# Optimization experiments

Measured on AMD Instinct MI355X. Metric: run time of the kernel, lower is better.

Reference implementation:

```python
import jax, jax.numpy as jnp
import numpy as np

BN_EPS = 1e-5

def _bn_relu(x, gamma, beta):
    # x: [B, C, N]; BatchNorm1d in training mode: stats over (B, N) per channel
    mean = jnp.mean(x, axis=(0, 2), keepdims=True)
    var = jnp.var(x, axis=(0, 2), keepdims=True)
    xn = (x - mean) * jax.lax.rsqrt(var + BN_EPS)
    return jax.nn.relu(xn * gamma[None, :, None] + beta[None, :, None])


def setup_inputs() -> dict:
    key = jax.random.key(0)
    ks = jax.random.split(key, 8)
    B, N, S, D1, D2 = 16, 4096, 1024, 64, 256
    C_in, H = D1 + D2, 256  # mlp_list = [320, 256, 256]
    inp = {
        "xyz1": jax.random.normal(ks[0], (B, 3, N), jnp.float32),
        "xyz2": jax.random.normal(ks[1], (B, 3, S), jnp.float32),
        "points1": jax.random.normal(ks[2], (B, D1, N), jnp.float32),
        "points2": jax.random.normal(ks[3], (B, D2, S), jnp.float32),
        # 1x1 Conv1d weights of the SeqLinear pointNet MLP
        "W1": jax.random.normal(ks[4], (H, C_in), jnp.float32) / np.sqrt(C_in),
        "b1": jnp.zeros((H,), jnp.float32),
        "g1": jnp.ones((H,), jnp.float32),
        "bt1": jnp.zeros((H,), jnp.float32),
        "W2": jax.random.normal(ks[5], (H, H), jnp.float32) / np.sqrt(H),
        "b2": jnp.zeros((H,), jnp.float32),
        "g2": jnp.ones((H,), jnp.float32),
        "bt2": jnp.zeros((H,), jnp.float32),
    }
    return inp


def reference(xyz1, xyz2, points1, points2, W1, b1, g1, bt1, W2, b2, g2, bt2):
    x1 = jnp.transpose(xyz1, (0, 2, 1))   # [B, N, 3]
    x2 = jnp.transpose(xyz2, (0, 2, 1))   # [B, S, 3]
    p2 = jnp.transpose(points2, (0, 2, 1))  # [B, S, D2]
    B, N, _ = x1.shape

    # square_distance: ||x1||^2 + ||x2||^2 - 2 x1.x2  -> [B, N, S]
    dists = (jnp.sum(x1 * x1, axis=-1, keepdims=True)
             + jnp.sum(x2 * x2, axis=-1)[:, None, :]
             - 2.0 * jnp.einsum('bnc,bsc->bns', x1, x2))

    # 3 nearest neighbors (smallest distances)
    neg_d3, idx = jax.lax.top_k(-dists, 3)   # [B, N, 3]
    d3 = -neg_d3
    recip = 1.0 / (d3 + 1e-8)
    weight = recip / jnp.sum(recip, axis=2, keepdims=True)  # [B, N, 3]

    # gather neighbor features: [B, N, 3, D2]
    gathered = jax.vmap(lambda p, i: p[i])(p2, idx)
    interp = jnp.sum(gathered * weight[..., None], axis=2)  # [B, N, D2]

    new_points = jnp.concatenate([jnp.transpose(points1, (0, 2, 1)), interp], axis=-1)
    x = jnp.transpose(new_points, (0, 2, 1))  # [B, 320, N]

    # pointNet MLP: conv1x1 -> BN -> ReLU, twice
    h = jnp.einsum('oc,bcn->bon', W1, x) + b1[None, :, None]
    h = _bn_relu(h, g1, bt1)
    h = jnp.einsum('oc,bcn->bon', W2, h) + b2[None, :, None]
    h = _bn_relu(h, g2, bt2)
    return h
```

## Files before the change

### kernel.cpp

```cpp
#include <hip/hip_runtime.h>
#include <cstddef>

#define B_   16
#define N_   4096
#define S_   1024
#define D1_  64
#define D2_  256
#define CIN_ 320
#define H_   256
#define CH_  8
#define SC_  (S_ / CH_)
#define P_   (B_ * (N_ / 128))

using short8 = __attribute__((ext_vector_type(8))) short;
using f32x4  = __attribute__((ext_vector_type(4))) float;

typedef const __attribute__((address_space(1))) unsigned g1u32;
typedef __attribute__((address_space(3))) unsigned l3u32;

__device__ __forceinline__ void gl_lds16(const void* g, void* l) {
  __builtin_amdgcn_global_load_lds((g1u32*)g, (l3u32*)l, 16, 0, 0);
}

__device__ __forceinline__ float relu_f(float v) { return fmaxf(v, 0.0f); }

__device__ __forceinline__ ushort f2bf(float f) {
  unsigned u = __builtin_bit_cast(unsigned, f);
  u += 0x7fffu + ((u >> 16) & 1u);
  return (ushort)(u >> 16);
}
__device__ __forceinline__ unsigned f2bf2(float a, float b) {
  unsigned r;
  asm("v_cvt_pk_bf16_f32 %0, %1, %2" : "=v"(r) : "v"(a), "v"(b));
  return r;
}
__device__ __forceinline__ float bf2f(ushort u) {
  return __builtin_bit_cast(float, (unsigned)u << 16);
}

__global__ __launch_bounds__(256) void prep_knn(
    const float* __restrict__ points2, const float* __restrict__ W1,
    const float* __restrict__ W2, const float* __restrict__ xyz1,
    const float* __restrict__ xyz2, ushort* __restrict__ p2tb,
    ushort* __restrict__ W1b, ushort* __restrict__ W2b,
    float* __restrict__ pd, int* __restrict__ pi) {
  __shared__ union { float tile[32][33]; float4 P[SC_]; } sm;
  int g = blockIdx.x, t = threadIdx.x;
  if (g < 4096) {
    int z = g >> 8, rem = g & 255;
    int c0 = (rem & 31) * 32;
    int r0 = (rem >> 5) * 32;
    const float* in = points2 + (size_t)z * D2_ * S_;
    ushort* out = p2tb + (size_t)z * S_ * D2_;
    int tx = t & 31, ty = t >> 5;
#pragma unroll
    for (int j = 0; j < 4; ++j) {
      int r = r0 + ty + j * 8;
      sm.tile[ty + j * 8][tx] = in[(size_t)r * S_ + c0 + tx];
    }
    __syncthreads();
#pragma unroll
    for (int j = 0; j < 4; ++j) {
      int c = c0 + ty + j * 8;
      out[(size_t)c * D2_ + r0 + tx] = f2bf(sm.tile[tx][ty + j * 8]);
    }
  } else if (g < 4168) {
    int g2 = g - 4096;
    const float* src = (g2 < 40) ? W1 : W2;
    ushort* dst = (g2 < 40) ? W1b : W2b;
    int base = ((g2 < 40) ? g2 : g2 - 40) * 2048 + t * 8;
    float4 a = *(const float4*)&src[base];
    float4 b = *(const float4*)&src[base + 4];
    short8 r;
    ((unsigned*)&r)[0] = f2bf2(a.x, a.y);
    ((unsigned*)&r)[1] = f2bf2(a.z, a.w);
    ((unsigned*)&r)[2] = f2bf2(b.x, b.y);
    ((unsigned*)&r)[3] = f2bf2(b.z, b.w);
    *(short8*)&dst[base] = r;
  } else {
    int gk = g - 4168;
    int b = gk & 15;
    int ch = (gk >> 4) & 7;
    int n = (gk >> 7) * 256 + t;
    const float* x2b = xyz2 + (size_t)b * 3 * S_ + ch * SC_;
    if (t < SC_) {
      float x = x2b[t], y = x2b[S_ + t], z = x2b[2 * S_ + t];
      sm.P[t] = make_float4(-2.f * x, -2.f * y, -2.f * z, x * x + y * y + z * z);
    }
    __syncthreads();

    const float* x1b = xyz1 + (size_t)b * 3 * N_;
    float px = x1b[n], py = x1b[N_ + n], pz = x1b[2 * N_ + n];
    float sq1 = px * px + py * py + pz * pz;

    float d0 = 1e30f, d1 = 1e30f, d2 = 1e30f;
    int i0 = 0, i1 = 0, i2 = 0;
#pragma unroll 4
    for (int s = 0; s < SC_; ++s) {
      float4 p = sm.P[s];
      float d = fmaf(px, p.x, fmaf(py, p.y, fmaf(pz, p.z, p.w)));
      int gi = ch * SC_ + s;
      if (d < d2) {
        if (d < d1) {
          if (d < d0) { d2 = d1; i2 = i1; d1 = d0; i1 = i0; d0 = d; i0 = gi; }
          else        { d2 = d1; i2 = i1; d1 = d;  i1 = gi; }
        } else        { d2 = d;  i2 = gi; }
      }
    }
    size_t base = (((size_t)b * N_ + n) * CH_ + ch) * 3;
    pd[base] = d0 + sq1; pd[base + 1] = d1 + sq1; pd[base + 2] = d2 + sq1;
    pi[base] = i0; pi[base + 1] = i1; pi[base + 2] = i2;
  }
}

__global__ __launch_bounds__(256) void build_fused(
    const float* __restrict__ points1,
    const ushort* __restrict__ p2tb,
    const float* __restrict__ pd, const int* __restrict__ pi,
    ushort* __restrict__ xt) {
  __shared__ int   lidx[16][3];
  __shared__ float lw[16][3];
  __shared__ ushort p1t[16][72];
  int g = blockIdx.x, t = threadIdx.x;
  int b = g & 15;
  int p0 = (g >> 4) * 16;

  if (t < 16) {
    size_t pb = (size_t)b * N_ + p0 + t;
    const float* pdp = pd + pb * 24;
    const int*   pip = pi + pb * 24;
    float d0 = 1e30f, d1 = 1e30f, d2 = 1e30f;
    int i0 = 0, i1 = 0, i2 = 0;
#pragma unroll
    for (int k = 0; k < 24; ++k) {
      float d = pdp[k];
      int gi = pip[k];
      if (d < d2) {
        if (d < d1) {
          if (d < d0) { d2 = d1; i2 = i1; d1 = d0; i1 = i0; d0 = d; i0 = gi; }
          else        { d2 = d1; i2 = i1; d1 = d;  i1 = gi; }
        } else        { d2 = d;  i2 = gi; }
      }
    }
    float r0 = 1.0f / (d0 + 1e-8f);
    float r1 = 1.0f / (d1 + 1e-8f);
    float r2 = 1.0f / (d2 + 1e-8f);
    float rs = 1.0f / (r0 + r1 + r2);
    lidx[t][0] = i0; lidx[t][1] = i1; lidx[t][2] = i2;
    lw[t][0] = r0 * rs; lw[t][1] = r1 * rs; lw[t][2] = r2 * rs;
  }

  {
    int c = t >> 2, q4 = t & 3;
    float4 v = *(const float4*)&points1[((size_t)b * D1_ + c) * N_ + p0 + q4 * 4];
    p1t[q4 * 4 + 0][c] = f2bf(v.x);
    p1t[q4 * 4 + 1][c] = f2bf(v.y);
    p1t[q4 * 4 + 2][c] = f2bf(v.z);
    p1t[q4 * 4 + 3][c] = f2bf(v.w);
  }
  __syncthreads();

  int pl = t >> 4, q = t & 15;
  size_t pb = (size_t)b * N_ + p0 + pl;
  int i0 = lidx[pl][0], i1 = lidx[pl][1], i2 = lidx[pl][2];
  float w0 = lw[pl][0], w1 = lw[pl][1], w2 = lw[pl][2];
  const ushort* R0 = p2tb + ((size_t)b * S_ + i0) * D2_;
  const ushort* R1 = p2tb + ((size_t)b * S_ + i1) * D2_;
  const ushort* R2 = p2tb + ((size_t)b * S_ + i2) * D2_;
  ushort* o = xt + pb * CIN_;

  if (q < 8)
    *(short8*)(o + q * 8) = *(const short8*)&p1t[pl][q * 8];

#pragma unroll
  for (int it = 0; it < 2; ++it) {
    int c = it * 16 + q;
    short8 a = *(const short8*)&R0[c * 8];
    short8 d = *(const short8*)&R1[c * 8];
    short8 e = *(const short8*)&R2[c * 8];
    short8 r;
#pragma unroll
    for (int u = 0; u < 4; ++u) {
      float v0 = w0 * bf2f((ushort)a[2 * u]) + w1 * bf2f((ushort)d[2 * u]) +
                 w2 * bf2f((ushort)e[2 * u]);
      float v1 = w0 * bf2f((ushort)a[2 * u + 1]) + w1 * bf2f((ushort)d[2 * u + 1]) +
                 w2 * bf2f((ushort)e[2 * u + 1]);
      ((unsigned*)&r)[u] = f2bf2(v0, v1);
    }
    *(short8*)(o + D1_ + c * 8) = r;
  }
}

template <int K, bool BNIN>
__global__ __launch_bounds__(256) void gemm_pipe(
    const ushort* __restrict__ Wb, const ushort* __restrict__ Xt,
    const float* __restrict__ bias, const float* __restrict__ scin,
    const float* __restrict__ shin, ushort* __restrict__ Yt,
    float* __restrict__ ps1, float* __restrict__ ps2) {
  constexpr int NT = K / 64;
  __shared__ union SM {
    struct { ushort A[2][128][64]; ushort Bt[2][128][64]; } st;
    struct { ushort C[128][132]; float S1[128][33]; float S2[128][33]; } ep;
  } sm;
  __shared__ float scs_l[H_], shs_l[H_];

  int b  = blockIdx.z;
  int n0 = blockIdx.x * 128;
  int m0 = blockIdx.y * 128;
  int tid = threadIdx.x;
  int lane = tid & 63, wid = tid >> 6;
  int wm = (wid >> 1) * 64, wn = (wid & 1) * 64;
  int lr = lane & 15, hi = lane >> 4;
  size_t bn0 = (size_t)b * N_ + n0;

  if (BNIN) {
    for (int i = tid; i < K; i += 256) { scs_l[i] = scin[i]; shs_l[i] = shin[i]; }
  }

  const char* Agb = (const char*)(Wb + (size_t)m0 * K);
  const ushort* Bg = Xt + bn0 * K;
  const char* Bgb = (const char*)Bg;
  const size_t rowB = (size_t)K * 2;

  size_t gsrc[4];
  int    ldst[4];
  int    brow[4], bcol[4];
#pragma unroll
  for (int r = 0; r < 4; ++r) {
    int m = (wid * 4 + r) * 64 + lane;
    int row = m >> 3;
    int c = ((m & 7) - row) & 7;
    gsrc[r] = (size_t)row * rowB + (size_t)c * 16;
    ldst[r] = m * 16;
    brow[r] = row; bcol[r] = c;
  }

  auto stageA = [&](int buf, int kc) {
    char* bA = (char*)sm.st.A[buf];
    size_t kb = (size_t)kc * 128;
#pragma unroll
    for (int r = 0; r < 4; ++r)
      gl_lds16(Agb + gsrc[r] + kb, bA + ldst[r]);
  };
  auto stageB_dma = [&](int buf, int kc) {
    char* bB = (char*)sm.st.Bt[buf];
    size_t kb = (size_t)kc * 128;
#pragma unroll
    for (int r = 0; r < 4; ++r)
      gl_lds16(Bgb + gsrc[r] + kb, bB + ldst[r]);
  };

  short8 braw[4];
  auto loadB = [&](int kc) {
#pragma unroll
    for (int r = 0; r < 4; ++r)
      braw[r] = *(const short8*)&Bg[(size_t)brow[r] * K + kc * 64 + bcol[r] * 8];
  };
  auto writeB = [&](int buf, int kc) {
#pragma unroll
    for (int r = 0; r < 4; ++r) {
      int kb = kc * 64 + bcol[r] * 8;
      short8 pk;
#pragma unroll
      for (int u = 0; u < 4; ++u) {
        float y0 = relu_f(bf2f((ushort)braw[r][2 * u]) * scs_l[kb + 2 * u] +
                          shs_l[kb + 2 * u]);
        float y1 = relu_f(bf2f((ushort)braw[r][2 * u + 1]) * scs_l[kb + 2 * u + 1] +
                          shs_l[kb + 2 * u + 1]);
        ((unsigned*)&pk)[u] = f2bf2(y0, y1);
      }
      *(short8*)((char*)sm.st.Bt[buf] + ldst[r]) = pk;
    }
  };

  f32x4 acc[4][4] = {};

  stageA(0, 0);
  if (BNIN) {
    loadB(0);
    __syncthreads();
    writeB(0, 0);
  } else {
    stageB_dma(0, 0);
  }
  __syncthreads();

  int cur = 0;
  for (int t = 0; t < NT; ++t) {
    if (t + 1 < NT) {
      stageA(cur ^ 1, t + 1);
      if (BNIN) loadB(t + 1); else stageB_dma(cur ^ 1, t + 1);
    }
#pragma unroll
    for (int ks = 0; ks < 2; ++ks) {
      short8 af[4], bv[4];
#pragma unroll
      for (int i = 0; i < 4; ++i) {
        int rA = wm + i * 16 + lr;
        int rB = wn + i * 16 + lr;
        int sA = (rA + ks * 4 + hi) & 7;
        int sB = (rB + ks * 4 + hi) & 7;
        af[i] = *(const short8*)&sm.st.A[cur][rA][sA * 8];
        bv[i] = *(const short8*)&sm.st.Bt[cur][rB][sB * 8];
      }
#pragma unroll
      for (int mf = 0; mf < 4; ++mf)
#pragma unroll
        for (int nf = 0; nf < 4; ++nf)
          acc[mf][nf] = __builtin_amdgcn_mfma_f32_16x16x32_bf16(
              af[mf], bv[nf], acc[mf][nf], 0, 0, 0);
    }
    if (BNIN && t + 1 < NT) writeB(cur ^ 1, t + 1);
    __syncthreads();
    cur ^= 1;
  }

  float sum1[4][4] = {}, sum2[4][4] = {};
#pragma unroll
  for (int mf = 0; mf < 4; ++mf) {
#pragma unroll
    for (int nf = 0; nf < 4; ++nf) {
      int n = wn + nf * 16 + lr;
      float v[4];
#pragma unroll
      for (int j = 0; j < 4; ++j) {
        v[j] = acc[mf][nf][j] + bias[m0 + wm + mf * 16 + hi * 4 + j];
        sum1[mf][j] += v[j];
        sum2[mf][j] += v[j] * v[j];
      }
      ushort4 u;
      ((unsigned*)&u)[0] = f2bf2(v[0], v[1]);
      ((unsigned*)&u)[1] = f2bf2(v[2], v[3]);
      *(ushort4*)&sm.ep.C[n][wm + mf * 16 + hi * 4] = u;
    }
  }
  __syncthreads();
  {
    int rown = tid >> 4, q = tid & 15;
#pragma unroll
    for (int p = 0; p < 8; ++p) {
      int n = p * 16 + rown;
      short8 val = *(const short8*)&sm.ep.C[n][q * 8];
      *(short8*)&Yt[(bn0 + n) * H_ + m0 + q * 8] = val;
    }
  }
  int col = (wid & 1) * 16 + lr;
#pragma unroll
  for (int mf = 0; mf < 4; ++mf)
#pragma unroll
    for (int j = 0; j < 4; ++j) {
      int c = wm + mf * 16 + hi * 4 + j;
      sm.ep.S1[c][col] = sum1[mf][j];
      sm.ep.S2[c][col] = sum2[mf][j];
    }
  __syncthreads();
  int pidx = b * gridDim.x + blockIdx.x;
  int c = tid & 127;
  float s = 0.f;
  if (tid < 128) {
#pragma unroll
    for (int k = 0; k < 32; ++k) s += sm.ep.S1[c][k];
    ps1[(size_t)pidx * H_ + m0 + c] = s;
  } else {
#pragma unroll
    for (int k = 0; k < 32; ++k) s += sm.ep.S2[c][k];
    ps2[(size_t)pidx * H_ + m0 + c] = s;
  }
}

__global__ __launch_bounds__(256) void bn_stats_fin(
    const float* __restrict__ ps1, const float* __restrict__ ps2,
    const float* __restrict__ gamma, const float* __restrict__ beta,
    float* __restrict__ sc, float* __restrict__ sh) {
  int c = blockIdx.x, t = threadIdx.x;
  float s1 = ps1[(size_t)t * H_ + c] + ps1[(size_t)(t + 256) * H_ + c];
  float s2 = ps2[(size_t)t * H_ + c] + ps2[(size_t)(t + 256) * H_ + c];
  __shared__ float S1[256], S2[256];
  S1[t] = s1; S2[t] = s2;
  __syncthreads();
  for (int off = 128; off > 0; off >>= 1) {
    if (t < off) { S1[t] += S1[t + off]; S2[t] += S2[t + off]; }
    __syncthreads();
  }
  if (t == 0) {
    const float inv = 1.0f / (float)(B_ * N_);
    float mean = S1[0] * inv;
    float var  = S2[0] * inv - mean * mean;
    float g    = gamma[c] * rsqrtf(var + 1e-5f);
    sc[c] = g;
    sh[c] = beta[c] - mean * g;
  }
}

__global__ __launch_bounds__(256) void bn_out_t(
    const ushort* __restrict__ Hb, const float* __restrict__ sc,
    const float* __restrict__ sh, float* __restrict__ out) {
  __shared__ float tile[32][132];
  int b = blockIdx.z;
  int n0 = blockIdx.x * 32, m0 = blockIdx.y * 128;
  int t = threadIdx.x;
  int m8 = (t & 15) * 8;
  f32x4 sa = *(const f32x4*)&sc[m0 + m8];
  f32x4 sb = *(const f32x4*)&sc[m0 + m8 + 4];
  f32x4 ha = *(const f32x4*)&sh[m0 + m8];
  f32x4 hb = *(const f32x4*)&sh[m0 + m8 + 4];
  size_t bn0 = (size_t)b * N_ + n0;
#pragma unroll
  for (int pass = 0; pass < 2; ++pass) {
    int n = pass * 16 + (t >> 4);
    short8 v = *(const short8*)&Hb[(bn0 + n) * H_ + m0 + m8];
#pragma unroll
    for (int e = 0; e < 4; ++e) {
      tile[n][m8 + e]     = relu_f(bf2f((ushort)v[e]) * sa[e] + ha[e]);
      tile[n][m8 + 4 + e] = relu_f(bf2f((ushort)v[e + 4]) * sb[e] + hb[e]);
    }
  }
  __syncthreads();
  int m = t >> 1, nh = (t & 1) * 16;
  float* orow = out + ((size_t)b * H_ + m0 + m) * N_ + n0 + nh;
#pragma unroll
  for (int j = 0; j < 4; ++j) {
    float4 v;
    v.x = tile[nh + j * 4 + 0][m];
    v.y = tile[nh + j * 4 + 1][m];
    v.z = tile[nh + j * 4 + 2][m];
    v.w = tile[nh + j * 4 + 3][m];
    *(float4*)&orow[j * 4] = v;
  }
}

extern "C" void kernel_launch(void* const* d_in, const int* in_sizes, int n_in,
                              void* d_out, int out_size, void* d_ws,
                              size_t ws_size, hipStream_t stream) {
  const float* xyz1    = (const float*)d_in[0];
  const float* xyz2    = (const float*)d_in[1];
  const float* points1 = (const float*)d_in[2];
  const float* points2 = (const float*)d_in[3];
  const float* W1  = (const float*)d_in[4];
  const float* b1  = (const float*)d_in[5];
  const float* g1  = (const float*)d_in[6];
  const float* bt1 = (const float*)d_in[7];
  const float* W2  = (const float*)d_in[8];
  const float* b2  = (const float*)d_in[9];
  const float* g2  = (const float*)d_in[10];
  const float* bt2 = (const float*)d_in[11];
  float* out = (float*)d_out;
  char* cur = (char*)d_ws;
  auto alloc = [&](size_t bytes) { char* p = cur; cur += (bytes + 255) & ~255ull; return p; };

  ushort* p2tb = (ushort*)alloc((size_t)B_ * S_ * D2_ * 2);
  float*  pd   = (float*)alloc((size_t)B_ * N_ * CH_ * 3 * 4);
  int*    pi   = (int*)alloc((size_t)B_ * N_ * CH_ * 3 * 4);
  ushort* W1b  = (ushort*)alloc((size_t)H_ * CIN_ * 2);
  ushort* W2b  = (ushort*)alloc((size_t)H_ * H_ * 2);
  ushort* xct  = (ushort*)alloc((size_t)B_ * N_ * CIN_ * 2);
  ushort* h1t  = (ushort*)alloc((size_t)B_ * N_ * H_ * 2);
  float*  ps1  = (float*)alloc((size_t)P_ * H_ * 4);
  float*  ps2  = (float*)alloc((size_t)P_ * H_ * 4);
  float*  sc1  = (float*)alloc(H_ * 4);
  float*  sh1  = (float*)alloc(H_ * 4);
  float*  sc2  = (float*)alloc(H_ * 4);
  float*  sh2  = (float*)alloc(H_ * 4);
  ushort* h2b  = xct;

  prep_knn<<<4096 + 40 + 32 + 2048, 256, 0, stream>>>(
      points2, W1, W2, xyz1, xyz2, p2tb, W1b, W2b, pd, pi);

  build_fused<<<B_ * N_ / 16, 256, 0, stream>>>(points1, p2tb, pd, pi, xct);

  gemm_pipe<CIN_, false><<<dim3(N_ / 128, H_ / 128, B_), 256, 0, stream>>>(
      W1b, xct, b1, nullptr, nullptr, h1t, ps1, ps2);
  bn_stats_fin<<<H_, 256, 0, stream>>>(ps1, ps2, g1, bt1, sc1, sh1);

  gemm_pipe<H_, true><<<dim3(N_ / 128, H_ / 128, B_), 256, 0, stream>>>(
      W2b, h1t, b2, sc1, sh1, h2b, ps1, ps2);
  bn_stats_fin<<<H_, 256, 0, stream>>>(ps1, ps2, g2, bt2, sc2, sh2);

  bn_out_t<<<dim3(N_ / 32, H_ / 128, B_), 256, 0, stream>>>(h2b, sc2, sh2, out);
}
```

Baseline: 154.7 us.

## Apply W1 to source features before interpolation and fuse gather into first GEMM

Since interpolation is linear, the change multiplies the D2 slice of W1 with points2 once per source point (S=1024 rows instead of N=4096) to form Z, then in a new fused kernel computes W1a·points1 with MFMA and adds the weighted three-neighbour sum of Z rows in the epilogue. This drops the separate build kernel and the large concatenated bf16 intermediate, cutting GEMM1 FLOPs and memory traffic. It adds an extra bf16 rounding of Z before interpolation, and switches grids to flat 1D indexing with batch as the fastest-varying index.

```diff
diff --git a/kernel.cpp b/kernel.cpp
--- a/kernel.cpp
+++ b/kernel.cpp
@@ -42,8 +42,8 @@
     const float* __restrict__ points2, const float* __restrict__ W1,
     const float* __restrict__ W2, const float* __restrict__ xyz1,
     const float* __restrict__ xyz2, ushort* __restrict__ p2tb,
-    ushort* __restrict__ W1b, ushort* __restrict__ W2b,
-    float* __restrict__ pd, int* __restrict__ pi) {
+    ushort* __restrict__ W1a, ushort* __restrict__ W1z,
+    ushort* __restrict__ W2b, float* __restrict__ pd, int* __restrict__ pi) {
   __shared__ union { float tile[32][33]; float4 P[SC_]; } sm;
   int g = blockIdx.x, t = threadIdx.x;
   if (g < 4096) {
@@ -66,17 +66,32 @@
     }
   } else if (g < 4168) {
     int g2 = g - 4096;
-    const float* src = (g2 < 40) ? W1 : W2;
-    ushort* dst = (g2 < 40) ? W1b : W2b;
-    int base = ((g2 < 40) ? g2 : g2 - 40) * 2048 + t * 8;
-    float4 a = *(const float4*)&src[base];
-    float4 b = *(const float4*)&src[base + 4];
+    const float* s;
+    ushort* dst;
+    int e;
+    if (g2 < 8) {
+      e = g2 * 2048 + t * 8;
+      int row = e >> 6, col = e & 63;
+      s = W1 + (size_t)row * CIN_ + col;
+      dst = W1a;
+    } else if (g2 < 40) {
+      e = (g2 - 8) * 2048 + t * 8;
+      int row = e >> 8, col = e & 255;
+      s = W1 + (size_t)row * CIN_ + 64 + col;
+      dst = W1z;
+    } else {
+      e = (g2 - 40) * 2048 + t * 8;
+      s = W2 + e;
+      dst = W2b;
+    }
+    float4 a = *(const float4*)s;
+    float4 b = *(const float4*)(s + 4);
     short8 r;
     ((unsigned*)&r)[0] = f2bf2(a.x, a.y);
     ((unsigned*)&r)[1] = f2bf2(a.z, a.w);
     ((unsigned*)&r)[2] = f2bf2(b.x, b.y);
     ((unsigned*)&r)[3] = f2bf2(b.z, b.w);
-    *(short8*)&dst[base] = r;
+    *(short8*)&dst[e] = r;
   } else {
     int gk = g - 4168;
     int b = gk & 15;
@@ -96,10 +111,10 @@
     float d0 = 1e30f, d1 = 1e30f, d2 = 1e30f;
     int i0 = 0, i1 = 0, i2 = 0;
 #pragma unroll 4
-    for (int s = 0; s < SC_; ++s) {
-      float4 p = sm.P[s];
+    for (int s2 = 0; s2 < SC_; ++s2) {
+      float4 p = sm.P[s2];
       float d = fmaf(px, p.x, fmaf(py, p.y, fmaf(pz, p.z, p.w)));
-      int gi = ch * SC_ + s;
+      int gi = ch * SC_ + s2;
       if (d < d2) {
         if (d < d1) {
           if (d < d0) { d2 = d1; i2 = i1; d1 = d0; i1 = i0; d0 = d; i0 = gi; }
@@ -113,85 +128,7 @@
   }
 }
 
-__global__ __launch_bounds__(256) void build_fused(
-    const float* __restrict__ points1,
-    const ushort* __restrict__ p2tb,
-    const float* __restrict__ pd, const int* __restrict__ pi,
-    ushort* __restrict__ xt) {
-  __shared__ int   lidx[16][3];
-  __shared__ float lw[16][3];
-  __shared__ ushort p1t[16][72];
-  int g = blockIdx.x, t = threadIdx.x;
-  int b = g & 15;
-  int p0 = (g >> 4) * 16;
-
-  if (t < 16) {
-    size_t pb = (size_t)b * N_ + p0 + t;
-    const float* pdp = pd + pb * 24;
-    const int*   pip = pi + pb * 24;
-    float d0 = 1e30f, d1 = 1e30f, d2 = 1e30f;
-    int i0 = 0, i1 = 0, i2 = 0;
-#pragma unroll
-    for (int k = 0; k < 24; ++k) {
-      float d = pdp[k];
-      int gi = pip[k];
-      if (d < d2) {
-        if (d < d1) {
-          if (d < d0) { d2 = d1; i2 = i1; d1 = d0; i1 = i0; d0 = d; i0 = gi; }
-          else        { d2 = d1; i2 = i1; d1 = d;  i1 = gi; }
-        } else        { d2 = d;  i2 = gi; }
-      }
-    }
-    float r0 = 1.0f / (d0 + 1e-8f);
-    float r1 = 1.0f / (d1 + 1e-8f);
-    float r2 = 1.0f / (d2 + 1e-8f);
-    float rs = 1.0f / (r0 + r1 + r2);
-    lidx[t][0] = i0; lidx[t][1] = i1; lidx[t][2] = i2;
-    lw[t][0] = r0 * rs; lw[t][1] = r1 * rs; lw[t][2] = r2 * rs;
-  }
-
-  {
-    int c = t >> 2, q4 = t & 3;
-    float4 v = *(const float4*)&points1[((size_t)b * D1_ + c) * N_ + p0 + q4 * 4];
-    p1t[q4 * 4 + 0][c] = f2bf(v.x);
-    p1t[q4 * 4 + 1][c] = f2bf(v.y);
-    p1t[q4 * 4 + 2][c] = f2bf(v.z);
-    p1t[q4 * 4 + 3][c] = f2bf(v.w);
-  }
-  __syncthreads();
-
-  int pl = t >> 4, q = t & 15;
-  size_t pb = (size_t)b * N_ + p0 + pl;
-  int i0 = lidx[pl][0], i1 = lidx[pl][1], i2 = lidx[pl][2];
-  float w0 = lw[pl][0], w1 = lw[pl][1], w2 = lw[pl][2];
-  const ushort* R0 = p2tb + ((size_t)b * S_ + i0) * D2_;
-  const ushort* R1 = p2tb + ((size_t)b * S_ + i1) * D2_;
-  const ushort* R2 = p2tb + ((size_t)b * S_ + i2) * D2_;
-  ushort* o = xt + pb * CIN_;
-
-  if (q < 8)
-    *(short8*)(o + q * 8) = *(const short8*)&p1t[pl][q * 8];
-
-#pragma unroll
-  for (int it = 0; it < 2; ++it) {
-    int c = it * 16 + q;
-    short8 a = *(const short8*)&R0[c * 8];
-    short8 d = *(const short8*)&R1[c * 8];
-    short8 e = *(const short8*)&R2[c * 8];
-    short8 r;
-#pragma unroll
-    for (int u = 0; u < 4; ++u) {
-      float v0 = w0 * bf2f((ushort)a[2 * u]) + w1 * bf2f((ushort)d[2 * u]) +
-                 w2 * bf2f((ushort)e[2 * u]);
-      float v1 = w0 * bf2f((ushort)a[2 * u + 1]) + w1 * bf2f((ushort)d[2 * u + 1]) +
-                 w2 * bf2f((ushort)e[2 * u + 1]);
-      ((unsigned*)&r)[u] = f2bf2(v0, v1);
-    }
-    *(short8*)(o + D1_ + c * 8) = r;
-  }
-}
-
-template <int K, bool BNIN>
+template <int K, int NN, bool BNIN, bool STATS>
 __global__ __launch_bounds__(256) void gemm_pipe(
     const ushort* __restrict__ Wb, const ushort* __restrict__ Xt,
     const float* __restrict__ bias, const float* __restrict__ scin,
@@ -204,14 +141,17 @@
   } sm;
   __shared__ float scs_l[H_], shs_l[H_];
 
-  int b  = blockIdx.z;
-  int n0 = blockIdx.x * 128;
-  int m0 = blockIdx.y * 128;
+  int g = blockIdx.x;
+  int b = g & 15;
+  int rr = g >> 4;
+  int m0 = (rr & 1) * 128;
+  int nb = rr >> 1;
+  int n0 = nb * 128;
   int tid = threadIdx.x;
   int lane = tid & 63, wid = tid >> 6;
   int wm = (wid >> 1) * 64, wn = (wid & 1) * 64;
   int lr = lane & 15, hi = lane >> 4;
-  size_t bn0 = (size_t)b * N_ + n0;
+  size_t bn0 = (size_t)b * NN + n0;
 
   if (BNIN) {
     for (int i = tid; i < K; i += 256) { scs_l[i] = scin[i]; shs_l[i] = shin[i]; }
@@ -324,9 +264,12 @@
       float v[4];
 #pragma unroll
       for (int j = 0; j < 4; ++j) {
-        v[j] = acc[mf][nf][j] + bias[m0 + wm + mf * 16 + hi * 4 + j];
-        sum1[mf][j] += v[j];
-        sum2[mf][j] += v[j] * v[j];
+        v[j] = acc[mf][nf][j];
+        if (STATS) {
+          v[j] += bias[m0 + wm + mf * 16 + hi * 4 + j];
+          sum1[mf][j] += v[j];
+          sum2[mf][j] += v[j] * v[j];
+        }
       }
       ushort4 u;
       ((unsigned*)&u)[0] = f2bf2(v[0], v[1]);
@@ -344,6 +287,180 @@
       *(short8*)&Yt[(bn0 + n) * H_ + m0 + q * 8] = val;
     }
   }
+  if (STATS) {
+    int col = (wid & 1) * 16 + lr;
+#pragma unroll
+    for (int mf = 0; mf < 4; ++mf)
+#pragma unroll
+      for (int j = 0; j < 4; ++j) {
+        int c = wm + mf * 16 + hi * 4 + j;
+        sm.ep.S1[c][col] = sum1[mf][j];
+        sm.ep.S2[c][col] = sum2[mf][j];
+      }
+    __syncthreads();
+    int pidx = b * (NN / 128) + nb;
+    int c = tid & 127;
+    float s = 0.f;
+    if (tid < 128) {
+#pragma unroll
+      for (int k = 0; k < 32; ++k) s += sm.ep.S1[c][k];
+      ps1[(size_t)pidx * H_ + m0 + c] = s;
+    } else {
+#pragma unroll
+      for (int k = 0; k < 32; ++k) s += sm.ep.S2[c][k];
+      ps2[(size_t)pidx * H_ + m0 + c] = s;
+    }
+  }
+}
+
+__global__ __launch_bounds__(256) void gemm_axz(
+    const ushort* __restrict__ Wa,
+    const float* __restrict__ points1,
+    const ushort* __restrict__ Z,
+    const float* __restrict__ pd, const int* __restrict__ pi,
+    const float* __restrict__ bias, ushort* __restrict__ Yt,
+    float* __restrict__ ps1, float* __restrict__ ps2) {
+  __shared__ union SM {
+    struct { ushort A[128][64]; ushort Bt[128][64]; } st;
+    struct { ushort C[128][132]; float S1[128][33]; float S2[128][33]; } ep;
+  } sm;
+  __shared__ int   lidx[128][3];
+  __shared__ float lw[128][3];
+
+  int g = blockIdx.x;
+  int b = g & 15;
+  int rr = g >> 4;
+  int m0 = (rr & 1) * 128;
+  int nb = rr >> 1;
+  int n0 = nb * 128;
+  int tid = threadIdx.x;
+  int lane = tid & 63, wid = tid >> 6;
+  int wm = (wid >> 1) * 64, wn = (wid & 1) * 64;
+  int lr = lane & 15, hi = lane >> 4;
+  size_t bn0 = (size_t)b * N_ + n0;
+
+  const char* Agb = (const char*)(Wa + (size_t)m0 * 64);
+#pragma unroll
+  for (int r = 0; r < 4; ++r) {
+    int m = (wid * 4 + r) * 64 + lane;
+    int row = m >> 3;
+    int c = ((m & 7) - row) & 7;
+    gl_lds16(Agb + (size_t)row * 128 + (size_t)c * 16, (char*)sm.st.A + m * 16);
+  }
+
+  {
+    int c = tid & 63, nq = tid >> 6;
+    const float* s1 = points1 + ((size_t)b * D1_ + c) * N_ + n0 + nq * 32;
+    int cc0 = c >> 3, ce = c & 7;
+#pragma unroll
+    for (int j = 0; j < 8; ++j) {
+      float4 v = *(const float4*)&s1[j * 4];
+      const float* vp = (const float*)&v;
+#pragma unroll
+      for (int e = 0; e < 4; ++e) {
+        int r = nq * 32 + j * 4 + e;
+        sm.st.Bt[r][(((r + cc0) & 7) << 3) + ce] = f2bf(vp[e]);
+      }
+    }
+  }
+
+  if (tid < 128) {
+    size_t pb = bn0 + tid;
+    const float* pdp = pd + pb * 24;
+    const int*   pip = pi + pb * 24;
+    float d0 = 1e30f, d1 = 1e30f, d2 = 1e30f;
+    int i0 = 0, i1 = 0, i2 = 0;
+#pragma unroll
+    for (int k = 0; k < 24; ++k) {
+      float d = pdp[k];
+      int gi = pip[k];
+      if (d < d2) {
+        if (d < d1) {
+          if (d < d0) { d2 = d1; i2 = i1; d1 = d0; i1 = i0; d0 = d; i0 = gi; }
+          else        { d2 = d1; i2 = i1; d1 = d;  i1 = gi; }
+        } else        { d2 = d;  i2 = gi; }
+      }
+    }
+    float r0 = 1.0f / (d0 + 1e-8f);
+    float r1 = 1.0f / (d1 + 1e-8f);
+    float r2 = 1.0f / (d2 + 1e-8f);
+    float rs = 1.0f / (r0 + r1 + r2);
+    lidx[tid][0] = i0; lidx[tid][1] = i1; lidx[tid][2] = i2;
+    lw[tid][0] = r0 * rs; lw[tid][1] = r1 * rs; lw[tid][2] = r2 * rs;
+  }
+  __syncthreads();
+
+  f32x4 acc[4][4] = {};
+#pragma unroll
+  for (int ks = 0; ks < 2; ++ks) {
+    short8 af[4], bv[4];
+#pragma unroll
+    for (int i = 0; i < 4; ++i) {
+      int rA = wm + i * 16 + lr;
+      int rB = wn + i * 16 + lr;
+      af[i] = *(const short8*)&sm.st.A[rA][((rA + ks * 4 + hi) & 7) * 8];
+      bv[i] = *(const short8*)&sm.st.Bt[rB][((rB + ks * 4 + hi) & 7) * 8];
+    }
+#pragma unroll
+    for (int mf = 0; mf < 4; ++mf)
+#pragma unroll
+      for (int nf = 0; nf < 4; ++nf)
+        acc[mf][nf] = __builtin_amdgcn_mfma_f32_16x16x32_bf16(
+            af[mf], bv[nf], acc[mf][nf], 0, 0, 0);
+  }
+
+  const ushort* Zb = Z + (size_t)b * S_ * H_;
+#pragma unroll
+  for (int nf = 0; nf < 4; ++nf) {
+    int nl = wn + nf * 16 + lr;
+    float w0 = lw[nl][0], w1 = lw[nl][1], w2 = lw[nl][2];
+    const ushort* z0 = Zb + (size_t)lidx[nl][0] * H_ + m0;
+    const ushort* z1 = Zb + (size_t)lidx[nl][1] * H_ + m0;
+    const ushort* z2 = Zb + (size_t)lidx[nl][2] * H_ + m0;
+#pragma unroll
+    for (int mf = 0; mf < 4; ++mf) {
+      int mo = wm + mf * 16 + hi * 4;
+      ushort4 a0 = *(const ushort4*)&z0[mo];
+      ushort4 a1 = *(const ushort4*)&z1[mo];
+      ushort4 a2 = *(const ushort4*)&z2[mo];
+#pragma unroll
+      for (int j = 0; j < 4; ++j)
+        acc[mf][nf][j] += w0 * bf2f(((const ushort*)&a0)[j]) +
+                          w1 * bf2f(((const ushort*)&a1)[j]) +
+                          w2 * bf2f(((const ushort*)&a2)[j]);
+    }
+  }
+  __syncthreads();
+
+  float sum1[4][4] = {}, sum2[4][4] = {};
+#pragma unroll
+  for (int mf = 0; mf < 4; ++mf) {
+#pragma unroll
+    for (int nf = 0; nf < 4; ++nf) {
+      int n = wn + nf * 16 + lr;
+      float v[4];
+#pragma unroll
+      for (int j = 0; j < 4; ++j) {
+        v[j] = acc[mf][nf][j] + bias[m0 + wm + mf * 16 + hi * 4 + j];
+        sum1[mf][j] += v[j];
+        sum2[mf][j] += v[j] * v[j];
+      }
+      ushort4 u;
+      ((unsigned*)&u)[0] = f2bf2(v[0], v[1]);
+      ((unsigned*)&u)[1] = f2bf2(v[2], v[3]);
+      *(ushort4*)&sm.ep.C[n][wm + mf * 16 + hi * 4] = u;
+    }
+  }
+  __syncthreads();
+  {
+    int rown = tid >> 4, q = tid & 15;
+#pragma unroll
+    for (int p = 0; p < 8; ++p) {
+      int n = p * 16 + rown;
+      short8 val = *(const short8*)&sm.ep.C[n][q * 8];
+      *(short8*)&Yt[(bn0 + n) * H_ + m0 + q * 8] = val;
+    }
+  }
   int col = (wid & 1) * 16 + lr;
 #pragma unroll
   for (int mf = 0; mf < 4; ++mf)
@@ -354,7 +471,7 @@
       sm.ep.S2[c][col] = sum2[mf][j];
     }
   __syncthreads();
-  int pidx = b * gridDim.x + blockIdx.x;
+  int pidx = b * 32 + nb;
   int c = tid & 127;
   float s = 0.f;
   if (tid < 128) {
@@ -396,8 +513,10 @@
     const ushort* __restrict__ Hb, const float* __restrict__ sc,
     const float* __restrict__ sh, float* __restrict__ out) {
   __shared__ float tile[32][132];
-  int b = blockIdx.z;
-  int n0 = blockIdx.x * 32, m0 = blockIdx.y * 128;
+  int g = blockIdx.x;
+  int b = g & 15;
+  int m0 = ((g >> 4) & 1) * 128;
+  int n0 = (g >> 5) * 32;
   int t = threadIdx.x;
   int m8 = (t & 15) * 8;
   f32x4 sa = *(const f32x4*)&sc[m0 + m8];
@@ -451,30 +570,32 @@
   ushort* p2tb = (ushort*)alloc((size_t)B_ * S_ * D2_ * 2);
   float*  pd   = (float*)alloc((size_t)B_ * N_ * CH_ * 3 * 4);
   int*    pi   = (int*)alloc((size_t)B_ * N_ * CH_ * 3 * 4);
-  ushort* W1b  = (ushort*)alloc((size_t)H_ * CIN_ * 2);
+  ushort* W1a  = (ushort*)alloc((size_t)H_ * D1_ * 2);
+  ushort* W1z  = (ushort*)alloc((size_t)H_ * D2_ * 2);
   ushort* W2b  = (ushort*)alloc((size_t)H_ * H_ * 2);
-  ushort* xct  = (ushort*)alloc((size_t)B_ * N_ * CIN_ * 2);
+  ushort* Zb_  = (ushort*)alloc((size_t)B_ * S_ * H_ * 2);
   ushort* h1t  = (ushort*)alloc((size_t)B_ * N_ * H_ * 2);
+  ushort* h2b  = (ushort*)alloc((size_t)B_ * N_ * H_ * 2);
   float*  ps1  = (float*)alloc((size_t)P_ * H_ * 4);
   float*  ps2  = (float*)alloc((size_t)P_ * H_ * 4);
   float*  sc1  = (float*)alloc(H_ * 4);
   float*  sh1  = (float*)alloc(H_ * 4);
   float*  sc2  = (float*)alloc(H_ * 4);
   float*  sh2  = (float*)alloc(H_ * 4);
-  ushort* h2b  = xct;
-
-  prep_knn<<<4096 + 40 + 32 + 2048, 256, 0, stream>>>(
-      points2, W1, W2, xyz1, xyz2, p2tb, W1b, W2b, pd, pi);
-
-  build_fused<<<B_ * N_ / 16, 256, 0, stream>>>(points1, p2tb, pd, pi, xct);
-
-  gemm_pipe<CIN_, false><<<dim3(N_ / 128, H_ / 128, B_), 256, 0, stream>>>(
-      W1b, xct, b1, nullptr, nullptr, h1t, ps1, ps2);
+
+  prep_knn<<<4096 + 72 + 2048, 256, 0, stream>>>(
+      points2, W1, W2, xyz1, xyz2, p2tb, W1a, W1z, W2b, pd, pi);
+
+  gemm_pipe<256, S_, false, false><<<256, 256, 0, stream>>>(
+      W1z, p2tb, nullptr, nullptr, nullptr, Zb_, nullptr, nullptr);
+
+  gemm_axz<<<1024, 256, 0, stream>>>(
+      W1a, points1, Zb_, pd, pi, b1, h1t, ps1, ps2);
   bn_stats_fin<<<H_, 256, 0, stream>>>(ps1, ps2, g1, bt1, sc1, sh1);
 
-  gemm_pipe<H_, true><<<dim3(N_ / 128, H_ / 128, B_), 256, 0, stream>>>(
+  gemm_pipe<256, N_, true, true><<<1024, 256, 0, stream>>>(
       W2b, h1t, b2, sc1, sh1, h2b, ps1, ps2);
   bn_stats_fin<<<H_, 256, 0, stream>>>(ps1, ps2, g2, bt2, sc2, sh2);
 
-  bn_out_t<<<dim3(N_ / 32, H_ / 128, B_), 256, 0, stream>>>(h2b, sc2, sh2, out);
-}
+  bn_out_t<<<4096, 256, 0, stream>>>(h2b, sc2, sh2, out);
+}
```

New measurement: 160.9 us. 1.04x slower.

## Single-buffer GEMM B tile through registers and split epilogue LDS union

Applied to the files above, without the earlier changes.

The GEMM kernel drops the double-buffered B tile in LDS and replaces it with one buffer. B is always loaded into registers and written after the MFMA loop, which adds an extra barrier per k-step, and the non-BN path no longer uses the direct global-to-LDS load. The epilogue union is split so the C staging buffer and the statistics buffers overlap, at the cost of one more barrier. The aim is to cut LDS use per block (roughly 64KB to about 48KB) to raise occupancy, but it gives up overlap of B writes with compute and adds synchronization.

```diff
diff --git a/kernel.cpp b/kernel.cpp
--- a/kernel.cpp
+++ b/kernel.cpp
@@ -96,10 +96,10 @@
     float d0 = 1e30f, d1 = 1e30f, d2 = 1e30f;
     int i0 = 0, i1 = 0, i2 = 0;
 #pragma unroll 4
-    for (int s = 0; s < SC_; ++s) {
-      float4 p = sm.P[s];
+    for (int s2 = 0; s2 < SC_; ++s2) {
+      float4 p = sm.P[s2];
       float d = fmaf(px, p.x, fmaf(py, p.y, fmaf(pz, p.z, p.w)));
-      int gi = ch * SC_ + s;
+      int gi = ch * SC_ + s2;
       if (d < d2) {
         if (d < d1) {
           if (d < d0) { d2 = d1; i2 = i1; d1 = d0; i1 = i0; d0 = d; i0 = gi; }
@@ -199,8 +199,9 @@
     float* __restrict__ ps1, float* __restrict__ ps2) {
   constexpr int NT = K / 64;
   __shared__ union SM {
-    struct { ushort A[2][128][64]; ushort Bt[2][128][64]; } st;
-    struct { ushort C[128][132]; float S1[128][33]; float S2[128][33]; } ep;
+    struct { ushort A[2][128][64]; ushort B1[128][64]; } st;
+    struct { ushort C[128][132]; } e1;
+    struct { float S1[128][33]; float S2[128][33]; } e2;
   } sm;
   __shared__ float scs_l[H_], shs_l[H_];
 
@@ -219,7 +220,6 @@
 
   const char* Agb = (const char*)(Wb + (size_t)m0 * K);
   const ushort* Bg = Xt + bn0 * K;
-  const char* Bgb = (const char*)Bg;
   const size_t rowB = (size_t)K * 2;
 
   size_t gsrc[4];
@@ -242,13 +242,6 @@
     for (int r = 0; r < 4; ++r)
       gl_lds16(Agb + gsrc[r] + kb, bA + ldst[r]);
   };
-  auto stageB_dma = [&](int buf, int kc) {
-    char* bB = (char*)sm.st.Bt[buf];
-    size_t kb = (size_t)kc * 128;
-#pragma unroll
-    for (int r = 0; r < 4; ++r)
-      gl_lds16(Bgb + gsrc[r] + kb, bB + ldst[r]);
-  };
 
   short8 braw[4];
   auto loadB = [&](int kc) {
@@ -256,40 +249,38 @@
     for (int r = 0; r < 4; ++r)
       braw[r] = *(const short8*)&Bg[(size_t)brow[r] * K + kc * 64 + bcol[r] * 8];
   };
-  auto writeB = [&](int buf, int kc) {
+  auto writeB = [&](int kc) {
 #pragma unroll
     for (int r = 0; r < 4; ++r) {
-      int kb = kc * 64 + bcol[r] * 8;
-      short8 pk;
-#pragma unroll
-      for (int u = 0; u < 4; ++u) {
-        float y0 = relu_f(bf2f((ushort)braw[r][2 * u]) * scs_l[kb + 2 * u] +
-                          shs_l[kb + 2 * u]);
-        float y1 = relu_f(bf2f((ushort)braw[r][2 * u + 1]) * scs_l[kb + 2 * u + 1] +
-                          shs_l[kb + 2 * u + 1]);
-        ((unsigned*)&pk)[u] = f2bf2(y0, y1);
+      short8 pk = braw[r];
+      if (BNIN) {
+        int kb = kc * 64 + bcol[r] * 8;
+#pragma unroll
+        for (int u = 0; u < 4; ++u) {
+          float y0 = relu_f(bf2f((ushort)braw[r][2 * u]) * scs_l[kb + 2 * u] +
+                            shs_l[kb + 2 * u]);
+          float y1 = relu_f(bf2f((ushort)braw[r][2 * u + 1]) * scs_l[kb + 2 * u + 1] +
+                            shs_l[kb + 2 * u + 1]);
+          ((unsigned*)&pk)[u] = f2bf2(y0, y1);
+        }
       }
-      *(short8*)((char*)sm.st.Bt[buf] + ldst[r]) = pk;
+      *(short8*)((char*)sm.st.B1 + ldst[r]) = pk;
     }
   };
 
   f32x4 acc[4][4] = {};
 
   stageA(0, 0);
-  if (BNIN) {
-    loadB(0);
-    __syncthreads();
-    writeB(0, 0);
-  } else {
-    stageB_dma(0, 0);
-  }
+  loadB(0);
+  __syncthreads();
+  writeB(0);
   __syncthreads();
 
   int cur = 0;
   for (int t = 0; t < NT; ++t) {
     if (t + 1 < NT) {
       stageA(cur ^ 1, t + 1);
-      if (BNIN) loadB(t + 1); else stageB_dma(cur ^ 1, t + 1);
+      loadB(t + 1);
     }
 #pragma unroll
     for (int ks = 0; ks < 2; ++ks) {
@@ -301,7 +292,7 @@
         int sA = (rA + ks * 4 + hi) & 7;
         int sB = (rB + ks * 4 + hi) & 7;
         af[i] = *(const short8*)&sm.st.A[cur][rA][sA * 8];
-        bv[i] = *(const short8*)&sm.st.Bt[cur][rB][sB * 8];
+        bv[i] = *(const short8*)&sm.st.B1[rB][sB * 8];
       }
 #pragma unroll
       for (int mf = 0; mf < 4; ++mf)
@@ -310,8 +301,11 @@
           acc[mf][nf] = __builtin_amdgcn_mfma_f32_16x16x32_bf16(
               af[mf], bv[nf], acc[mf][nf], 0, 0, 0);
     }
-    if (BNIN && t + 1 < NT) writeB(cur ^ 1, t + 1);
     __syncthreads();
+    if (t + 1 < NT) {
+      writeB(t + 1);
+      __syncthreads();
+    }
     cur ^= 1;
   }
 
@@ -331,7 +325,7 @@
       ushort4 u;
       ((unsigned*)&u)[0] = f2bf2(v[0], v[1]);
       ((unsigned*)&u)[1] = f2bf2(v[2], v[3]);
-      *(ushort4*)&sm.ep.C[n][wm + mf * 16 + hi * 4] = u;
+      *(ushort4*)&sm.e1.C[n][wm + mf * 16 + hi * 4] = u;
     }
   }
   __syncthreads();
@@ -340,18 +334,20 @@
 #pragma unroll
     for (int p = 0; p < 8; ++p) {
       int n = p * 16 + rown;
-      short8 val = *(const short8*)&sm.ep.C[n][q * 8];
+      short8 val = *(const short8*)&sm.e1.C[n][q * 8];
       *(short8*)&Yt[(bn0 + n) * H_ + m0 + q * 8] = val;
     }
   }
+  __syncthreads();
+
   int col = (wid & 1) * 16 + lr;
 #pragma unroll
   for (int mf = 0; mf < 4; ++mf)
 #pragma unroll
     for (int j = 0; j < 4; ++j) {
       int c = wm + mf * 16 + hi * 4 + j;
-      sm.ep.S1[c][col] = sum1[mf][j];
-      sm.ep.S2[c][col] = sum2[mf][j];
+      sm.e2.S1[c][col] = sum1[mf][j];
+      sm.e2.S2[c][col] = sum2[mf][j];
     }
   __syncthreads();
   int pidx = b * gridDim.x + blockIdx.x;
@@ -359,11 +355,11 @@
   float s = 0.f;
   if (tid < 128) {
 #pragma unroll
-    for (int k = 0; k < 32; ++k) s += sm.ep.S1[c][k];
+    for (int k = 0; k < 32; ++k) s += sm.e2.S1[c][k];
     ps1[(size_t)pidx * H_ + m0 + c] = s;
   } else {
 #pragma unroll
-    for (int k = 0; k < 32; ++k) s += sm.ep.S2[c][k];
+    for (int k = 0; k < 32; ++k) s += sm.e2.S2[c][k];
     ps2[(size_t)pidx * H_ + m0 + c] = s;
   }
 }
```

New measurement: 163.4 us. 5.6% more time.
